# Optimization experiments

Hardware: AMD Instinct MI355X
Metric: run time of the kernel (lower is better)

## Reference

```python
import jax, jax.numpy as jnp
import numpy as np
import math

H, HD = 16, 64
EPS = 1e-6


def setup_inputs() -> dict:
    key = jax.random.key(0)
    ks = jax.random.split(key, 6)
    B, T, D = 4, 2048, 1024
    s = 0.02
    return {
        "x": jax.random.normal(ks[0], (B, T, D), jnp.float32),
        "wq": jax.random.normal(ks[1], (D, D), jnp.float32) * s,
        "wk": jax.random.normal(ks[2], (D, D), jnp.float32) * s,
        "wv": jax.random.normal(ks[3], (D, D), jnp.float32) * s,
        "wo": jax.random.normal(ks[4], (D, D), jnp.float32) * s,
        "norm_g": jnp.ones((D,), jnp.float32),
    }


def reference(x, wq, wk, wv, wo, norm_g):
    B, T, D = x.shape
    scale = math.sqrt(HD)
    # nn.Linear(D, D, bias=False): y = x @ W.T
    q = (x @ wq.T).reshape(B, T, H, HD).transpose(0, 2, 1, 3)  # [B,H,T,HD]
    k = (x @ wk.T).reshape(B, T, H, HD).transpose(0, 2, 1, 3)
    v = (x @ wv.T).reshape(B, T, H, HD).transpose(0, 2, 1, 3)
    scores = jnp.einsum("bhqd,bhkd->bhqk", q, k) / scale  # [B,H,T,T]
    causal = jnp.tril(jnp.ones((T, T), bool))  # True where allowed
    scores = jnp.where(causal, scores, -jnp.inf)
    attn = jax.nn.softmax(scores, axis=-1)  # dropout p=0 -> identity
    out = jnp.einsum("bhqk,bhkd->bhqd", attn, v)  # [B,H,T,HD]
    out = out.transpose(0, 2, 1, 3).reshape(B, T, D)
    y = x + out @ wo.T  # residual
    # RMSNorm
    rms = jnp.sqrt(jnp.mean(y * y, axis=-1, keepdims=True) + EPS)
    return (y / rms) * norm_g
```

## Files before the change

### kernel.cpp

```cpp
#include <hip/hip_runtime.h>
#include <hip/hip_bf16.h>

constexpr int NB  = 4;
constexpr int NT  = 2048;
constexpr int ND  = 1024;
constexpr int NH  = 16;
constexpr int NHD = 64;
constexpr int NM  = NB * NT;

typedef unsigned short u16;
typedef __attribute__((ext_vector_type(8))) short  short8;
typedef __attribute__((ext_vector_type(4))) float  f32x4;

__device__ __forceinline__ u16 f2bf(float f) {
  unsigned u = __builtin_bit_cast(unsigned, f);
  u += 0x7FFFu + ((u >> 16) & 1u);
  return (u16)(u >> 16);
}

__device__ __forceinline__ unsigned pk2bf(float lo, float hi_) {
  float2 t; t.x = lo; t.y = hi_;
  __hip_bfloat162 h2 = __float22bfloat162_rn(t);
  unsigned u;
  __builtin_memcpy(&u, &h2, 4);
  return u;
}

__device__ __forceinline__ void gll16(const u16* src, u16* dst) {
  __builtin_amdgcn_global_load_lds(
      (const __attribute__((address_space(1))) void*)src,
      (__attribute__((address_space(3))) void*)dst, 16, 0, 0);
}

__global__ __launch_bounds__(256) void cast_all(
    const float* __restrict__ x,
    const float* __restrict__ w0, const float* __restrict__ w1,
    const float* __restrict__ w2, const float* __restrict__ w3,
    u16* __restrict__ xb,
    u16* __restrict__ o0, u16* __restrict__ o1,
    u16* __restrict__ o2, u16* __restrict__ o3) {
  const int bid = blockIdx.x;
  const float* in;
  u16* out;
  int i;
  if (bid < 8192) {
    in = x; out = xb; i = bid * 256 + threadIdx.x;
  } else {
    const int z = (bid - 8192) >> 10;
    in  = (z == 0) ? w0 : (z == 1) ? w1 : (z == 2) ? w2 : w3;
    out = (z == 0) ? o0 : (z == 1) ? o1 : (z == 2) ? o2 : o3;
    i = ((bid - 8192) & 1023) * 256 + threadIdx.x;
  }
  float4 v = ((const float4*)in)[i];
  ushort4 o;
  o.x = f2bf(v.x); o.y = f2bf(v.y); o.z = f2bf(v.z); o.w = f2bf(v.w);
  ((ushort4*)out)[i] = o;
}

__global__ __launch_bounds__(512, 2) void gemm_qkv3(
    const u16* __restrict__ xb,
    const u16* __restrict__ wqb, const u16* __restrict__ wkb, const u16* __restrict__ wvb,
    u16* __restrict__ Qb, u16* __restrict__ Kb, u16* __restrict__ VTb) {
  const int z    = blockIdx.z;
  const int row0 = blockIdx.x << 7;
  const int col0 = blockIdx.y << 7;

  const u16* wsel = (z == 0) ? wqb : (z == 1) ? wkb : wvb;
  u16* osel      = (z == 0) ? Qb  : (z == 1) ? Kb  : VTb;
  const float scl = (z == 0) ? 0.125f * 1.44269504f : 1.0f;

  const int tid  = threadIdx.x;
  const int lane = tid & 63, wid = tid >> 6;
  const int wm = wid >> 2, wn = wid & 3;
  const int li = lane & 15, hi = lane >> 4;
  const int l3 = lane >> 3, sl = lane & 7;
  const int schunk = ((sl ^ l3) << 3);

  extern __shared__ __align__(16) u16 smem[];
  u16* lAb = smem;
  u16* lBb = smem + 3 * 128 * 64;

  auto stage = [&](int t) {
    const int bo = (t % 3) * 8192;
    const int k0 = t << 6;
#pragma unroll
    for (int h = 0; h < 2; ++h) {
      int r = h * 64 + wid * 8;
      gll16(&xb  [(size_t)(row0 + r + l3) * ND + k0 + schunk], &lAb[bo + r * 64]);
      gll16(&wsel[(size_t)(col0 + r + l3) * ND + k0 + schunk], &lBb[bo + r * 64]);
    }
  };

  f32x4 acc[4][2] = {};

  stage(0);
  stage(1);

  for (int i = 0; i < 16; ++i) {
    if (i < 15) { asm volatile("s_waitcnt vmcnt(4)" ::: "memory"); }
    else        { asm volatile("s_waitcnt vmcnt(0)" ::: "memory"); }
    __builtin_amdgcn_s_barrier();

    if (i + 2 < 16) stage(i + 2);

    const u16* la = &lAb[(i % 3) * 8192];
    const u16* lb = &lBb[(i % 3) * 8192];

    short8 a[4][2], b[2][2];
#pragma unroll
    for (int m = 0; m < 4; ++m)
#pragma unroll
      for (int c = 0; c < 2; ++c)
        a[m][c] = *(const short8*)&la[(wm * 64 + m * 16 + li) * 64 + (((c * 4 + hi) ^ (li & 7)) << 3)];
#pragma unroll
    for (int n = 0; n < 2; ++n)
#pragma unroll
      for (int c = 0; c < 2; ++c)
        b[n][c] = *(const short8*)&lb[(wn * 32 + n * 16 + li) * 64 + (((c * 4 + hi) ^ (li & 7)) << 3)];

    if (z == 2) {
#pragma unroll
      for (int m = 0; m < 4; ++m)
#pragma unroll
        for (int n = 0; n < 2; ++n)
#pragma unroll
          for (int c = 0; c < 2; ++c)
            acc[m][n] = __builtin_amdgcn_mfma_f32_16x16x32_bf16(a[m][c], b[n][c], acc[m][n], 0, 0, 0);
    } else {
#pragma unroll
      for (int m = 0; m < 4; ++m)
#pragma unroll
        for (int n = 0; n < 2; ++n)
#pragma unroll
          for (int c = 0; c < 2; ++c)
            acc[m][n] = __builtin_amdgcn_mfma_f32_16x16x32_bf16(b[n][c], a[m][c], acc[m][n], 0, 0, 0);
    }
  }

#pragma unroll
  for (int m = 0; m < 4; ++m)
#pragma unroll
    for (int n = 0; n < 2; ++n) {
      if (z == 2) {
        int token0 = row0 + wm * 64 + m * 16 + hi * 4;
        int col    = col0 + wn * 32 + n * 16 + li;
        int b_ = token0 >> 11, t0 = token0 & (NT - 1);
        int h_ = col >> 6,     d_ = col & (NHD - 1);
        uint2 w;
        w.x = pk2bf(acc[m][n][0], acc[m][n][1]);
        w.y = pk2bf(acc[m][n][2], acc[m][n][3]);
        *(uint2*)&osel[(((size_t)(b_ * NH + h_)) * NHD + d_) * NT + t0] = w;
      } else {
        int token = row0 + wm * 64 + m * 16 + li;
        int feat0 = col0 + wn * 32 + n * 16 + hi * 4;
        int b_ = token >> 11, t_ = token & (NT - 1);
        int h_ = feat0 >> 6,  d0 = feat0 & (NHD - 1);
        uint2 w;
        w.x = pk2bf(acc[m][n][0] * scl, acc[m][n][1] * scl);
        w.y = pk2bf(acc[m][n][2] * scl, acc[m][n][3] * scl);
        *(uint2*)&osel[(((size_t)(b_ * NH + h_)) * NT + t_) * NHD + d0] = w;
      }
    }
}

__global__ __launch_bounds__(512, 2) void gemm_wo3(
    const u16* __restrict__ ao, const u16* __restrict__ wob,
    const float* __restrict__ x, float* __restrict__ y) {
  const int row0 = blockIdx.x << 7;
  const int col0 = blockIdx.y << 7;

  const int tid  = threadIdx.x;
  const int lane = tid & 63, wid = tid >> 6;
  const int wm = wid >> 2, wn = wid & 3;
  const int li = lane & 15, hi = lane >> 4;
  const int l3 = lane >> 3, sl = lane & 7;
  const int schunk = ((sl ^ l3) << 3);

  extern __shared__ __align__(16) u16 smem[];
  u16* lAb = smem;
  u16* lBb = smem + 3 * 128 * 64;

  auto stage = [&](int t) {
    const int bo = (t % 3) * 8192;
    const int k0 = t << 6;
#pragma unroll
    for (int h = 0; h < 2; ++h) {
      int r = h * 64 + wid * 8;
      gll16(&ao [(size_t)(row0 + r + l3) * ND + k0 + schunk], &lAb[bo + r * 64]);
      gll16(&wob[(size_t)(col0 + r + l3) * ND + k0 + schunk], &lBb[bo + r * 64]);
    }
  };

  f32x4 acc[4][2] = {};

  stage(0);
  stage(1);

  for (int i = 0; i < 16; ++i) {
    if (i < 15) { asm volatile("s_waitcnt vmcnt(4)" ::: "memory"); }
    else        { asm volatile("s_waitcnt vmcnt(0)" ::: "memory"); }
    __builtin_amdgcn_s_barrier();

    if (i + 2 < 16) stage(i + 2);

    const u16* la = &lAb[(i % 3) * 8192];
    const u16* lb = &lBb[(i % 3) * 8192];

    short8 a[4][2], b[2][2];
#pragma unroll
    for (int m = 0; m < 4; ++m)
#pragma unroll
      for (int c = 0; c < 2; ++c)
        a[m][c] = *(const short8*)&la[(wm * 64 + m * 16 + li) * 64 + (((c * 4 + hi) ^ (li & 7)) << 3)];
#pragma unroll
    for (int n = 0; n < 2; ++n)
#pragma unroll
      for (int c = 0; c < 2; ++c)
        b[n][c] = *(const short8*)&lb[(wn * 32 + n * 16 + li) * 64 + (((c * 4 + hi) ^ (li & 7)) << 3)];

#pragma unroll
    for (int m = 0; m < 4; ++m)
#pragma unroll
      for (int n = 0; n < 2; ++n)
#pragma unroll
        for (int c = 0; c < 2; ++c)
          acc[m][n] = __builtin_amdgcn_mfma_f32_16x16x32_bf16(b[n][c], a[m][c], acc[m][n], 0, 0, 0);
  }

#pragma unroll
  for (int m = 0; m < 4; ++m)
#pragma unroll
    for (int n = 0; n < 2; ++n) {
      int token = row0 + wm * 64 + m * 16 + li;
      int feat0 = col0 + wn * 32 + n * 16 + hi * 4;
      size_t idx = (size_t)token * ND + feat0;
      float4 xv = *(const float4*)&x[idx];
      float4 o;
      o.x = acc[m][n][0] + xv.x; o.y = acc[m][n][1] + xv.y;
      o.z = acc[m][n][2] + xv.z; o.w = acc[m][n][3] + xv.w;
      *(float4*)&y[idx] = o;
    }
}

__global__ __launch_bounds__(256) void attn_kernel(
    const u16* __restrict__ Q, const u16* __restrict__ K, const u16* __restrict__ VT,
    u16* __restrict__ AO) {
  const int nb  = gridDim.x * gridDim.y;
  const int b0  = blockIdx.y * gridDim.x + blockIdx.x;
  const int L   = (b0 & 7) * (nb >> 3) + (b0 >> 3);
  const int qb  = 31 - (L & 31);
  const int bh  = L >> 5;

  const int tid = threadIdx.x;
  const int lane = tid & 63, wid = tid >> 6;
  const int li = lane & 15, hi = lane >> 4;
  const int r0 = qb * 64 + wid * 16;
  const int qrow = r0 + li;
  const size_t bK = (size_t)bh * NT * NHD;
  const size_t bV = (size_t)bh * NHD * NT;

  __shared__ __align__(16) u16 lK [2][64 * 64];
  __shared__ __align__(16) u16 lVT[3][64 * 64];
  __shared__ __align__(16) u16 lP [4][16 * 64];

  const int ch0 = tid, ch1 = tid + 256;
  const int d0 = (ch0 >> 3) * 64 + (((ch0 & 7) ^ ((ch0 >> 3) & 7)) << 3);
  const int d1 = (ch1 >> 3) * 64 + (((ch1 & 7) ^ ((ch1 >> 3) & 7)) << 3);
  const int vOff0 = (ch0 >> 3) * NT + (ch0 & 7) * 8;
  const int vOff1 = (ch1 >> 3) * NT + (ch1 & 7) * 8;

  uint4 gK0, gK1, gV0, gV1;
  auto issue = [&](int kt) {
    const u16* kp = K + bK + (size_t)kt * 4096;
    const u16* vp = VT + bV + kt * 64;
    gK0 = *(const uint4*)&kp[ch0 * 8];
    gK1 = *(const uint4*)&kp[ch1 * 8];
    gV0 = *(const uint4*)&vp[vOff0];
    gV1 = *(const uint4*)&vp[vOff1];
  };
  auto commit = [&](int kt) {
    *(uint4*)&lK [kt & 1][d0] = gK0;
    *(uint4*)&lK [kt & 1][d1] = gK1;
    *(uint4*)&lVT[kt % 3][d0] = gV0;
    *(uint4*)&lVT[kt % 3][d1] = gV1;
  };

  short8 qf[2];
#pragma unroll
  for (int c = 0; c < 2; ++c)
    qf[c] = *(const short8*)&Q[bK + (size_t)qrow * NHD + c * 32 + hi * 8];

  short8 vone;
#pragma unroll
  for (int e = 0; e < 8; ++e) vone[e] = (short)0x3F80;

  f32x4 o[4] = {};
  f32x4 o4 = {};
  short8 pap0, pap1;

  issue(0);
  commit(0);
  __syncthreads();

  const int pswz = (li & 7) << 1;

  for (int kt = 0; kt <= qb; ++kt) {
    if (kt < qb) issue(kt + 1);

    f32x4 s[4] = {};
    __builtin_amdgcn_s_setprio(1);
#pragma unroll
    for (int g = 0; g < 4; ++g)
#pragma unroll
      for (int c = 0; c < 2; ++c) {
        short8 kf = *(const short8*)&lK[kt & 1][(g * 16 + li) * 64 + ((c * 4 + hi) ^ (li & 7)) * 8];
        s[g] = __builtin_amdgcn_mfma_f32_16x16x32_bf16(kf, qf[c], s[g], 0, 0, 0);
      }

    if (kt > 0) {
      const u16* lv = lVT[(kt - 1) % 3];
#pragma unroll
      for (int gd = 0; gd < 4; ++gd) {
        short8 vf0 = *(const short8*)&lv[(gd * 16 + li) * 64 + ((0 * 4 + hi) ^ (li & 7)) * 8];
        short8 vf1 = *(const short8*)&lv[(gd * 16 + li) * 64 + ((1 * 4 + hi) ^ (li & 7)) * 8];
        o[gd] = __builtin_amdgcn_mfma_f32_16x16x32_bf16(vf0, pap0, o[gd], 0, 0, 0);
        o[gd] = __builtin_amdgcn_mfma_f32_16x16x32_bf16(vf1, pap1, o[gd], 0, 0, 0);
      }
      o4 = __builtin_amdgcn_mfma_f32_16x16x32_bf16(vone, pap0, o4, 0, 0, 0);
      o4 = __builtin_amdgcn_mfma_f32_16x16x32_bf16(vone, pap1, o4, 0, 0, 0);
    }
    __builtin_amdgcn_s_setprio(0);

    if (kt == qb) {
#pragma unroll
      for (int g = 0; g < 4; ++g)
#pragma unroll
        for (int rg = 0; rg < 4; ++rg) {
          int kcol = kt * 64 + g * 16 + hi * 4 + rg;
          if (kcol > qrow) s[g][rg] = -INFINITY;
        }
    }

#pragma unroll
    for (int g = 0; g < 4; ++g) {
      float p0 = __builtin_amdgcn_exp2f(s[g][0]);
      float p1 = __builtin_amdgcn_exp2f(s[g][1]);
      float p2 = __builtin_amdgcn_exp2f(s[g][2]);
      float p3 = __builtin_amdgcn_exp2f(s[g][3]);
      uint2 w;
      w.x = pk2bf(p0, p1);
      w.y = pk2bf(p2, p3);
      int k8s = (g * 4 + hi) ^ pswz;
      *(uint2*)&lP[wid][li * 64 + k8s * 4] = w;
    }

    pap0 = *(const short8*)&lP[wid][li * 64 + ((0 * 8 + hi * 2) ^ pswz) * 4];
    pap1 = *(const short8*)&lP[wid][li * 64 + ((1 * 8 + hi * 2) ^ pswz) * 4];

    if (kt < qb) commit(kt + 1);
    __syncthreads();
  }

  {
    const u16* lv = lVT[qb % 3];
#pragma unroll
    for (int gd = 0; gd < 4; ++gd) {
      short8 vf0 = *(const short8*)&lv[(gd * 16 + li) * 64 + ((0 * 4 + hi) ^ (li & 7)) * 8];
      short8 vf1 = *(const short8*)&lv[(gd * 16 + li) * 64 + ((1 * 4 + hi) ^ (li & 7)) * 8];
      o[gd] = __builtin_amdgcn_mfma_f32_16x16x32_bf16(vf0, pap0, o[gd], 0, 0, 0);
      o[gd] = __builtin_amdgcn_mfma_f32_16x16x32_bf16(vf1, pap1, o[gd], 0, 0, 0);
    }
    o4 = __builtin_amdgcn_mfma_f32_16x16x32_bf16(vone, pap0, o4, 0, 0, 0);
    o4 = __builtin_amdgcn_mfma_f32_16x16x32_bf16(vone, pap1, o4, 0, 0, 0);
  }

  const int b_ = bh >> 4, h_ = bh & 15;
  const float inv = 1.0f / o4[0];
  const size_t rowbase = ((size_t)(b_ * NT + qrow)) * ND + h_ * 64;
#pragma unroll
  for (int gd = 0; gd < 4; ++gd) {
    uint2 w;
    w.x = pk2bf(o[gd][0] * inv, o[gd][1] * inv);
    w.y = pk2bf(o[gd][2] * inv, o[gd][3] * inv);
    *(uint2*)&AO[rowbase + gd * 16 + hi * 4] = w;
  }
}

__global__ __launch_bounds__(256) void rmsnorm_kernel(float* __restrict__ y,
                                                      const float* __restrict__ g) {
  const int row = blockIdx.x;
  const int tid = threadIdx.x;
  const int lane = tid & 63, wid = tid >> 6;
  float4 v = ((const float4*)(y + (size_t)row * ND))[tid];
  float ss = v.x * v.x + v.y * v.y + v.z * v.z + v.w * v.w;
#pragma unroll
  for (int off = 32; off; off >>= 1) ss += __shfl_down(ss, off);
  __shared__ float red[4];
  if (lane == 0) red[wid] = ss;
  __syncthreads();
  float tot = red[0] + red[1] + red[2] + red[3];
  float inv = rsqrtf(tot * (1.0f / (float)ND) + 1e-6f);
  float4 gg = ((const float4*)g)[tid];
  float4 o;
  o.x = v.x * inv * gg.x; o.y = v.y * inv * gg.y;
  o.z = v.z * inv * gg.z; o.w = v.w * inv * gg.w;
  ((float4*)(y + (size_t)row * ND))[tid] = o;
}

extern "C" void kernel_launch(void* const* d_in, const int* in_sizes, int n_in,
                              void* d_out, int out_size, void* d_ws, size_t ws_size,
                              hipStream_t stream) {
  const float* x  = (const float*)d_in[0];
  const float* wq = (const float*)d_in[1];
  const float* wk = (const float*)d_in[2];
  const float* wv = (const float*)d_in[3];
  const float* wo = (const float*)d_in[4];
  const float* ng = (const float*)d_in[5];
  float* out = (float*)d_out;

  char* ws = (char*)d_ws;
  u16* xb  = (u16*)(ws);
  u16* wqb = (u16*)(ws + (16u << 20));
  u16* wkb = (u16*)(ws + (18u << 20));
  u16* wvb = (u16*)(ws + (20u << 20));
  u16* wob = (u16*)(ws + (22u << 20));
  u16* Qb  = (u16*)(ws + (24u << 20));
  u16* Kb  = (u16*)(ws + (40u << 20));
  u16* VTb = (u16*)(ws + (56u << 20));
  u16* AO  = (u16*)(ws + (72u << 20));

  cast_all<<<8192 + 4096, 256, 0, stream>>>(x, wq, wk, wv, wo, xb, wqb, wkb, wvb, wob);

  gemm_qkv3<<<dim3(64, 8, 3), 512, 98304, stream>>>(xb, wqb, wkb, wvb, Qb, Kb, VTb);
  attn_kernel<<<dim3(NT / 64, NB * NH), 256, 0, stream>>>(Qb, Kb, VTb, AO);
  gemm_wo3<<<dim3(64, 8), 512, 98304, stream>>>(AO, wob, x, out);
  rmsnorm_kernel<<<NM, 256, 0, stream>>>(out, ng);
}
```

Measured before the change: 200.3 us.

## Enlarge attention query tile to 128 rows with 8 waves sharing K/V loads

The attention kernel now processes 128 query rows per block using 512 threads (8 waves), so each K/V tile staged in LDS is reused by twice as many query rows and the grid is halved. Waves whose rows lie entirely before a key tile skip its QK and PV work through per-wave active flags, and the causal mask is applied on the last two tiles. This cuts redundant global K/V traffic and per-block overhead. The cost is fewer blocks, more idle waves on the diagonal tiles, and coarser load balance across the causal triangle.

```diff
diff --git a/kernel.cpp b/kernel.cpp
--- a/kernel.cpp
+++ b/kernel.cpp
@@ -242,47 +242,39 @@
     }
 }
 
-__global__ __launch_bounds__(256) void attn_kernel(
+__global__ __launch_bounds__(512) void attn_kernel(
     const u16* __restrict__ Q, const u16* __restrict__ K, const u16* __restrict__ VT,
     u16* __restrict__ AO) {
   const int nb  = gridDim.x * gridDim.y;
   const int b0  = blockIdx.y * gridDim.x + blockIdx.x;
   const int L   = (b0 & 7) * (nb >> 3) + (b0 >> 3);
-  const int qb  = 31 - (L & 31);
-  const int bh  = L >> 5;
+  const int qs  = 15 - (L & 15);
+  const int bh  = L >> 4;
 
   const int tid = threadIdx.x;
   const int lane = tid & 63, wid = tid >> 6;
   const int li = lane & 15, hi = lane >> 4;
-  const int r0 = qb * 64 + wid * 16;
+  const int r0 = qs * 128 + wid * 16;
   const int qrow = r0 + li;
   const size_t bK = (size_t)bh * NT * NHD;
   const size_t bV = (size_t)bh * NHD * NT;
 
   __shared__ __align__(16) u16 lK [2][64 * 64];
   __shared__ __align__(16) u16 lVT[3][64 * 64];
-  __shared__ __align__(16) u16 lP [4][16 * 64];
-
-  const int ch0 = tid, ch1 = tid + 256;
-  const int d0 = (ch0 >> 3) * 64 + (((ch0 & 7) ^ ((ch0 >> 3) & 7)) << 3);
-  const int d1 = (ch1 >> 3) * 64 + (((ch1 & 7) ^ ((ch1 >> 3) & 7)) << 3);
-  const int vOff0 = (ch0 >> 3) * NT + (ch0 & 7) * 8;
-  const int vOff1 = (ch1 >> 3) * NT + (ch1 & 7) * 8;
-
-  uint4 gK0, gK1, gV0, gV1;
+  __shared__ __align__(16) u16 lP [8][16 * 64];
+
+  const int ch = tid;
+  const int dd   = (ch >> 3) * 64 + (((ch & 7) ^ ((ch >> 3) & 7)) << 3);
+  const int vOff = (ch >> 3) * NT + (ch & 7) * 8;
+
+  uint4 gK0, gV0;
   auto issue = [&](int kt) {
-    const u16* kp = K + bK + (size_t)kt * 4096;
-    const u16* vp = VT + bV + kt * 64;
-    gK0 = *(const uint4*)&kp[ch0 * 8];
-    gK1 = *(const uint4*)&kp[ch1 * 8];
-    gV0 = *(const uint4*)&vp[vOff0];
-    gV1 = *(const uint4*)&vp[vOff1];
+    gK0 = *(const uint4*)&K [bK + (size_t)kt * 4096 + ch * 8];
+    gV0 = *(const uint4*)&VT[bV + (size_t)kt * 64 + vOff];
   };
   auto commit = [&](int kt) {
-    *(uint4*)&lK [kt & 1][d0] = gK0;
-    *(uint4*)&lK [kt & 1][d1] = gK1;
-    *(uint4*)&lVT[kt % 3][d0] = gV0;
-    *(uint4*)&lVT[kt % 3][d1] = gV1;
+    *(uint4*)&lK [kt & 1][dd] = gK0;
+    *(uint4*)&lVT[kt % 3][dd] = gV0;
   };
 
   short8 qf[2];
@@ -296,28 +288,34 @@
 
   f32x4 o[4] = {};
   f32x4 o4 = {};
-  short8 pap0, pap1;
+  short8 pap0 = {}, pap1 = {};
+  bool prevAct = false;
 
   issue(0);
   commit(0);
   __syncthreads();
 
+  const int nkt = 2 * qs + 2;
   const int pswz = (li & 7) << 1;
 
-  for (int kt = 0; kt <= qb; ++kt) {
-    if (kt < qb) issue(kt + 1);
+  for (int kt = 0; kt < nkt; ++kt) {
+    if (kt + 1 < nkt) issue(kt + 1);
+
+    const bool act = (kt * 64 <= r0 + 15);
 
     f32x4 s[4] = {};
     __builtin_amdgcn_s_setprio(1);
-#pragma unroll
-    for (int g = 0; g < 4; ++g)
-#pragma unroll
-      for (int c = 0; c < 2; ++c) {
-        short8 kf = *(const short8*)&lK[kt & 1][(g * 16 + li) * 64 + ((c * 4 + hi) ^ (li & 7)) * 8];
-        s[g] = __builtin_amdgcn_mfma_f32_16x16x32_bf16(kf, qf[c], s[g], 0, 0, 0);
-      }
-
-    if (kt > 0) {
+    if (act) {
+#pragma unroll
+      for (int g = 0; g < 4; ++g)
+#pragma unroll
+        for (int c = 0; c < 2; ++c) {
+          short8 kf = *(const short8*)&lK[kt & 1][(g * 16 + li) * 64 + ((c * 4 + hi) ^ (li & 7)) * 8];
+          s[g] = __builtin_amdgcn_mfma_f32_16x16x32_bf16(kf, qf[c], s[g], 0, 0, 0);
+        }
+    }
+
+    if (prevAct) {
       const u16* lv = lVT[(kt - 1) % 3];
 #pragma unroll
       for (int gd = 0; gd < 4; ++gd) {
@@ -331,38 +329,41 @@
     }
     __builtin_amdgcn_s_setprio(0);
 
-    if (kt == qb) {
-#pragma unroll
-      for (int g = 0; g < 4; ++g)
-#pragma unroll
-        for (int rg = 0; rg < 4; ++rg) {
-          int kcol = kt * 64 + g * 16 + hi * 4 + rg;
-          if (kcol > qrow) s[g][rg] = -INFINITY;
-        }
-    }
-
-#pragma unroll
-    for (int g = 0; g < 4; ++g) {
-      float p0 = __builtin_amdgcn_exp2f(s[g][0]);
-      float p1 = __builtin_amdgcn_exp2f(s[g][1]);
-      float p2 = __builtin_amdgcn_exp2f(s[g][2]);
-      float p3 = __builtin_amdgcn_exp2f(s[g][3]);
-      uint2 w;
-      w.x = pk2bf(p0, p1);
-      w.y = pk2bf(p2, p3);
-      int k8s = (g * 4 + hi) ^ pswz;
-      *(uint2*)&lP[wid][li * 64 + k8s * 4] = w;
-    }
-
-    pap0 = *(const short8*)&lP[wid][li * 64 + ((0 * 8 + hi * 2) ^ pswz) * 4];
-    pap1 = *(const short8*)&lP[wid][li * 64 + ((1 * 8 + hi * 2) ^ pswz) * 4];
-
-    if (kt < qb) commit(kt + 1);
+    if (act) {
+      if (kt >= nkt - 2) {
+#pragma unroll
+        for (int g = 0; g < 4; ++g)
+#pragma unroll
+          for (int rg = 0; rg < 4; ++rg) {
+            int kcol = kt * 64 + g * 16 + hi * 4 + rg;
+            if (kcol > qrow) s[g][rg] = -INFINITY;
+          }
+      }
+
+#pragma unroll
+      for (int g = 0; g < 4; ++g) {
+        float p0 = __builtin_amdgcn_exp2f(s[g][0]);
+        float p1 = __builtin_amdgcn_exp2f(s[g][1]);
+        float p2 = __builtin_amdgcn_exp2f(s[g][2]);
+        float p3 = __builtin_amdgcn_exp2f(s[g][3]);
+        uint2 w;
+        w.x = pk2bf(p0, p1);
+        w.y = pk2bf(p2, p3);
+        int k8s = (g * 4 + hi) ^ pswz;
+        *(uint2*)&lP[wid][li * 64 + k8s * 4] = w;
+      }
+
+      pap0 = *(const short8*)&lP[wid][li * 64 + ((0 * 8 + hi * 2) ^ pswz) * 4];
+      pap1 = *(const short8*)&lP[wid][li * 64 + ((1 * 8 + hi * 2) ^ pswz) * 4];
+    }
+    prevAct = act;
+
+    if (kt + 1 < nkt) commit(kt + 1);
     __syncthreads();
   }
 
-  {
-    const u16* lv = lVT[qb % 3];
+  if (prevAct) {
+    const u16* lv = lVT[(nkt - 1) % 3];
 #pragma unroll
     for (int gd = 0; gd < 4; ++gd) {
       short8 vf0 = *(const short8*)&lv[(gd * 16 + li) * 64 + ((0 * 4 + hi) ^ (li & 7)) * 8];
@@ -432,7 +433,7 @@
   cast_all<<<8192 + 4096, 256, 0, stream>>>(x, wq, wk, wv, wo, xb, wqb, wkb, wvb, wob);
 
   gemm_qkv3<<<dim3(64, 8, 3), 512, 98304, stream>>>(xb, wqb, wkb, wvb, Qb, Kb, VTb);
-  attn_kernel<<<dim3(NT / 64, NB * NH), 256, 0, stream>>>(Qb, Kb, VTb, AO);
+  attn_kernel<<<dim3(16, NB * NH), 512, 0, stream>>>(Qb, Kb, VTb, AO);
   gemm_wo3<<<dim3(64, 8), 512, 98304, stream>>>(AO, wob, x, out);
   rmsnorm_kernel<<<NM, 256, 0, stream>>>(out, ng);
 }
```

New measurement: 205.8 us. 1.03x slower.

## Fuse Q/K/V projections into one kernel sharing the x tile

Applied to the files above, without the earlier changes.

Replaces the three-way grid-z QKV GEMM with one kernel in which each block loads the x tile once and multiplies it against the Wq, Wk and Wv tiles, keeping three accumulator sets. The goal is to cut redundant global and LDS traffic for x and reuse each A fragment across three MFMA groups. In exchange the pipeline drops from triple to double buffering with a full vmcnt(0) wait each iteration, LDS grows to 128KB per block, and accumulator register pressure triples. That lowers occupancy: with 128KB per block, likely only one block fits per CU, and the grid shrinks to 512 blocks, which may leave compute units underused.

```diff
diff --git a/kernel.cpp b/kernel.cpp
--- a/kernel.cpp
+++ b/kernel.cpp
@@ -57,17 +57,13 @@
   ((ushort4*)out)[i] = o;
 }
 
-__global__ __launch_bounds__(512, 2) void gemm_qkv3(
+__global__ __launch_bounds__(512, 2) void gemm_qkvm(
     const u16* __restrict__ xb,
     const u16* __restrict__ wqb, const u16* __restrict__ wkb, const u16* __restrict__ wvb,
     u16* __restrict__ Qb, u16* __restrict__ Kb, u16* __restrict__ VTb) {
-  const int z    = blockIdx.z;
   const int row0 = blockIdx.x << 7;
   const int col0 = blockIdx.y << 7;
-
-  const u16* wsel = (z == 0) ? wqb : (z == 1) ? wkb : wvb;
-  u16* osel      = (z == 0) ? Qb  : (z == 1) ? Kb  : VTb;
-  const float scl = (z == 0) ? 0.125f * 1.44269504f : 1.0f;
+  const float scl = 0.125f * 1.44269504f;
 
   const int tid  = threadIdx.x;
   const int lane = tid & 63, wid = tid >> 6;
@@ -77,88 +73,107 @@
   const int schunk = ((sl ^ l3) << 3);
 
   extern __shared__ __align__(16) u16 smem[];
-  u16* lAb = smem;
-  u16* lBb = smem + 3 * 128 * 64;
+  u16* lA = smem;
+  u16* lB = smem + 2 * 128 * 64;
 
   auto stage = [&](int t) {
-    const int bo = (t % 3) * 8192;
+    const int bf = t & 1;
     const int k0 = t << 6;
 #pragma unroll
     for (int h = 0; h < 2; ++h) {
       int r = h * 64 + wid * 8;
-      gll16(&xb  [(size_t)(row0 + r + l3) * ND + k0 + schunk], &lAb[bo + r * 64]);
-      gll16(&wsel[(size_t)(col0 + r + l3) * ND + k0 + schunk], &lBb[bo + r * 64]);
+      size_t go = (size_t)(col0 + r + l3) * ND + k0 + schunk;
+      gll16(&xb [(size_t)(row0 + r + l3) * ND + k0 + schunk], &lA[bf * 8192 + r * 64]);
+      gll16(&wqb[go], &lB[(bf * 3 + 0) * 8192 + r * 64]);
+      gll16(&wkb[go], &lB[(bf * 3 + 1) * 8192 + r * 64]);
+      gll16(&wvb[go], &lB[(bf * 3 + 2) * 8192 + r * 64]);
     }
   };
 
-  f32x4 acc[4][2] = {};
+  f32x4 acc[3][4][2] = {};
 
   stage(0);
-  stage(1);
+  asm volatile("s_waitcnt vmcnt(0)" ::: "memory");
+  __builtin_amdgcn_s_barrier();
 
   for (int i = 0; i < 16; ++i) {
-    if (i < 15) { asm volatile("s_waitcnt vmcnt(4)" ::: "memory"); }
-    else        { asm volatile("s_waitcnt vmcnt(0)" ::: "memory"); }
-    __builtin_amdgcn_s_barrier();
-
-    if (i + 2 < 16) stage(i + 2);
-
-    const u16* la = &lAb[(i % 3) * 8192];
-    const u16* lb = &lBb[(i % 3) * 8192];
-
-    short8 a[4][2], b[2][2];
+    if (i + 1 < 16) stage(i + 1);
+
+    const u16* la = &lA[(i & 1) * 8192];
+
+    short8 a[4][2];
 #pragma unroll
     for (int m = 0; m < 4; ++m)
 #pragma unroll
       for (int c = 0; c < 2; ++c)
         a[m][c] = *(const short8*)&la[(wm * 64 + m * 16 + li) * 64 + (((c * 4 + hi) ^ (li & 7)) << 3)];
-#pragma unroll
-    for (int n = 0; n < 2; ++n)
-#pragma unroll
-      for (int c = 0; c < 2; ++c)
-        b[n][c] = *(const short8*)&lb[(wn * 32 + n * 16 + li) * 64 + (((c * 4 + hi) ^ (li & 7)) << 3)];
-
-    if (z == 2) {
-#pragma unroll
-      for (int m = 0; m < 4; ++m)
-#pragma unroll
-        for (int n = 0; n < 2; ++n)
-#pragma unroll
-          for (int c = 0; c < 2; ++c)
-            acc[m][n] = __builtin_amdgcn_mfma_f32_16x16x32_bf16(a[m][c], b[n][c], acc[m][n], 0, 0, 0);
-    } else {
-#pragma unroll
-      for (int m = 0; m < 4; ++m)
-#pragma unroll
-        for (int n = 0; n < 2; ++n)
-#pragma unroll
-          for (int c = 0; c < 2; ++c)
-            acc[m][n] = __builtin_amdgcn_mfma_f32_16x16x32_bf16(b[n][c], a[m][c], acc[m][n], 0, 0, 0);
-    }
+
+#pragma unroll
+    for (int z = 0; z < 3; ++z) {
+      const u16* lb = &lB[((i & 1) * 3 + z) * 8192];
+      short8 b[2][2];
+#pragma unroll
+      for (int n = 0; n < 2; ++n)
+#pragma unroll
+        for (int c = 0; c < 2; ++c)
+          b[n][c] = *(const short8*)&lb[(wn * 32 + n * 16 + li) * 64 + (((c * 4 + hi) ^ (li & 7)) << 3)];
+
+      if (z == 2) {
+#pragma unroll
+        for (int m = 0; m < 4; ++m)
+#pragma unroll
+          for (int n = 0; n < 2; ++n)
+#pragma unroll
+            for (int c = 0; c < 2; ++c)
+              acc[z][m][n] = __builtin_amdgcn_mfma_f32_16x16x32_bf16(a[m][c], b[n][c], acc[z][m][n], 0, 0, 0);
+      } else {
+#pragma unroll
+        for (int m = 0; m < 4; ++m)
+#pragma unroll
+          for (int n = 0; n < 2; ++n)
+#pragma unroll
+            for (int c = 0; c < 2; ++c)
+              acc[z][m][n] = __builtin_amdgcn_mfma_f32_16x16x32_bf16(b[n][c], a[m][c], acc[z][m][n], 0, 0, 0);
+      }
+    }
+
+    if (i + 1 < 16) { asm volatile("s_waitcnt vmcnt(0)" ::: "memory"); }
+    __builtin_amdgcn_s_barrier();
   }
 
 #pragma unroll
   for (int m = 0; m < 4; ++m)
 #pragma unroll
     for (int n = 0; n < 2; ++n) {
-      if (z == 2) {
+      {
+        int token = row0 + wm * 64 + m * 16 + li;
+        int feat0 = col0 + wn * 32 + n * 16 + hi * 4;
+        int b_ = token >> 11, t_ = token & (NT - 1);
+        int h_ = feat0 >> 6,  d0 = feat0 & (NHD - 1);
+        uint2 w;
+        w.x = pk2bf(acc[0][m][n][0] * scl, acc[0][m][n][1] * scl);
+        w.y = pk2bf(acc[0][m][n][2] * scl, acc[0][m][n][3] * scl);
+        *(uint2*)&Qb[(((size_t)(b_ * NH + h_)) * NT + t_) * NHD + d0] = w;
+      }
+      {
+        int token = row0 + wm * 64 + m * 16 + li;
+        int feat0 = col0 + wn * 32 + n * 16 + hi * 4;
+        int b_ = token >> 11, t_ = token & (NT - 1);
+        int h_ = feat0 >> 6,  d0 = feat0 & (NHD - 1);
+        uint2 w;
+        w.x = pk2bf(acc[1][m][n][0], acc[1][m][n][1]);
+        w.y = pk2bf(acc[1][m][n][2], acc[1][m][n][3]);
+        *(uint2*)&Kb[(((size_t)(b_ * NH + h_)) * NT + t_) * NHD + d0] = w;
+      }
+      {
         int token0 = row0 + wm * 64 + m * 16 + hi * 4;
         int col    = col0 + wn * 32 + n * 16 + li;
         int b_ = token0 >> 11, t0 = token0 & (NT - 1);
         int h_ = col >> 6,     d_ = col & (NHD - 1);
         uint2 w;
-        w.x = pk2bf(acc[m][n][0], acc[m][n][1]);
-        w.y = pk2bf(acc[m][n][2], acc[m][n][3]);
-        *(uint2*)&osel[(((size_t)(b_ * NH + h_)) * NHD + d_) * NT + t0] = w;
-      } else {
-        int token = row0 + wm * 64 + m * 16 + li;
-        int feat0 = col0 + wn * 32 + n * 16 + hi * 4;
-        int b_ = token >> 11, t_ = token & (NT - 1);
-        int h_ = feat0 >> 6,  d0 = feat0 & (NHD - 1);
-        uint2 w;
-        w.x = pk2bf(acc[m][n][0] * scl, acc[m][n][1] * scl);
-        w.y = pk2bf(acc[m][n][2] * scl, acc[m][n][3] * scl);
-        *(uint2*)&osel[(((size_t)(b_ * NH + h_)) * NT + t_) * NHD + d0] = w;
+        w.x = pk2bf(acc[2][m][n][0], acc[2][m][n][1]);
+        w.y = pk2bf(acc[2][m][n][2], acc[2][m][n][3]);
+        *(uint2*)&VTb[(((size_t)(b_ * NH + h_)) * NHD + d_) * NT + t0] = w;
       }
     }
 }
@@ -431,7 +446,7 @@
 
   cast_all<<<8192 + 4096, 256, 0, stream>>>(x, wq, wk, wv, wo, xb, wqb, wkb, wvb, wob);
 
-  gemm_qkv3<<<dim3(64, 8, 3), 512, 98304, stream>>>(xb, wqb, wkb, wvb, Qb, Kb, VTb);
+  gemm_qkvm<<<dim3(64, 8), 512, 131072, stream>>>(xb, wqb, wkb, wvb, Qb, Kb, VTb);
   attn_kernel<<<dim3(NT / 64, NB * NH), 256, 0, stream>>>(Qb, Kb, VTb, AO);
   gemm_wo3<<<dim3(64, 8), 512, 98304, stream>>>(AO, wob, x, out);
   rmsnorm_kernel<<<NM, 256, 0, stream>>>(out, ng);
```

After: 183.5 us (median of 3 runs). 8.4% less time.
